# Performance work log

Hardware: AMD Instinct MI355X
Metric: run time of the kernel (lower is better)

## Reference

```python
import jax, jax.numpy as jnp
import numpy as np

B, N, D = 512, 256, 128
N_LAYER, N_HEAD = 4, 1
VAR = 0.01
HEAD = 0  # head_choice in run_mode=0


def setup_inputs() -> dict:
    key = jax.random.key(0)
    k1, k2 = jax.random.split(key)
    Z = jax.random.normal(k1, (B, N + 1, D + 1), dtype=jnp.float32)
    # allparam ~ N(0, var): torch .normal_(0, var) uses var as stddev
    allparam = jax.random.normal(k2, (N_LAYER, N_HEAD, 2, D, D), dtype=jnp.float32) * VAR
    gamma = jnp.ones((N_LAYER, N_HEAD, 1, N + 1, D + 1), dtype=jnp.float32)
    return {"Z": Z, "allparam": allparam, "gamma": gamma}


def _pad_full(M, corner):
    # Embed d x d matrix in (d+1) x (d+1) with zeros; set bottom-right corner.
    d = M.shape[0]
    full = jnp.zeros((d + 1, d + 1), M.dtype).at[:d, :d].set(M)
    return full.at[d, d].set(corner)


def _attention(P, Q, Z):
    # Z: [B, N+1, d+1]
    n = Z.shape[1] - 1
    P_full = _pad_full(P, 1.0)   # P with 1 at [d, d]
    Q_full = _pad_full(Q, 0.0)
    Attn = jnp.einsum('bni,ij,bmj->bnm', Z, Q_full, Z)  # [B, N+1, N+1]
    key = jnp.einsum('ij,bnj->bni', P_full, Z)           # [B, N+1, d+1]
    # A = eye(N+1) with A[N, N] = 0  <=>  zero the last token's key row
    key = key.at[:, n, :].set(0.0)
    return jnp.einsum('bnm,bmi->bni', Attn, key) / n


def reference(Z, allparam, gamma):
    # run_mode=0, chosen head = HEAD
    # T_i = R_i + sum_{k<i} R_k * gamma_k ; Z <- Z + T_i
    acc = jnp.zeros_like(Z)  # running sum_{k<i} R_k * gamma_k
    for i in range(N_LAYER):
        P = allparam[i, HEAD, 0]
        Q = allparam[i, HEAD, 1]
        R = _attention(P, Q, Z)
        T = R + acc
        acc = acc + R * gamma[i, HEAD, 0]
        Z = Z + T
    return Z
```

## Files before the change

kernel.cpp:

```cpp
#include <hip/hip_runtime.h>
#include <hip/hip_bf16.h>
#include <stdint.h>


using short8 = __attribute__((ext_vector_type(8))) short;
using f32x4  = __attribute__((ext_vector_type(4))) float;

#define MFMA16(A,B,C) __builtin_amdgcn_mfma_f32_16x16x32_bf16((A),(B),(C),0,0,0)

static __device__ __forceinline__ uint16_t f2bf(float f){
  union{__hip_bfloat16 h;uint16_t u;}c; c.h=__float2bfloat16(f); return c.u; }
static __device__ __forceinline__ uint32_t pk2(float lo,float hi){
  return (uint32_t)f2bf(lo) | ((uint32_t)f2bf(hi)<<16); }
static __device__ __forceinline__ float bfu(uint16_t u){ return __uint_as_float(((uint32_t)u)<<16); }
static __device__ __forceinline__ float bflo(uint32_t p){ return __uint_as_float(p<<16); }
static __device__ __forceinline__ float bfhi(uint32_t p){ return __uint_as_float(p&0xffff0000u); }

union F4 { uint32_t u[4]; short8 s8; };

#define ZTP   264
#define BUFP  152
#define SCRP  40
#define ZT_OFF   0
#define GBA_OFF  67584
#define GBB_OFF  106496
#define SCR_OFF  145408
#define ZBAR_OFF 155648
#define Z256_OFF 156688
#define A128_OFF 157200
#define A256_OFF 158224
#define G_OFF    158752
#define M1_OFF   159264
#define LDS_TOTAL 159776

__global__ __launch_bounds__(512)
__attribute__((amdgpu_waves_per_eu(2, 2)))
void tf_layers(const float* __restrict__ Zin, const float* __restrict__ gamma,
               const uint16_t* __restrict__ Qg, const uint16_t* __restrict__ Pg,
               float* __restrict__ Zout)
{
  extern __shared__ char lds[];
  uint16_t* ZT    = (uint16_t*)(lds + ZT_OFF);
  uint16_t* GbA   = (uint16_t*)(lds + GBA_OFF);
  uint16_t* GbB   = (uint16_t*)(lds + GBB_OFF);
  float*    zbar  = (float*)(lds + ZBAR_OFF);
  float*    z256f = (float*)(lds + Z256_OFF);
  float*    acc128= (float*)(lds + A128_OFF);
  float*    acc256= (float*)(lds + A256_OFF);
  float*    gv    = (float*)(lds + G_OFF);
  float*    m1v   = (float*)(lds + M1_OFF);

  const int tid = threadIdx.x, lane = tid & 63, w = tid >> 6;
  const int l15 = lane & 15, g4 = lane >> 4;
  const int b = blockIdx.x;
  const float inv_n = 1.0f/256.0f;

  uint16_t* scr = (uint16_t*)(lds + SCR_OFF) + w * 16 * SCRP;

  const float* Zb = Zin + (size_t)b*33153;
  float*       Zo = Zout + (size_t)b*33153;

  uint4* accb = (uint4*)(((uintptr_t)Zo + 15) & ~(uintptr_t)15);

  for (int i2 = tid; i2 < 33153; i2 += 512) {
    int r = i2/129, c = i2 - r*129;
    float v = Zb[i2];
    if (c < 128) { if (r < 256) ZT[c*ZTP + r] = f2bf(v); else z256f[c] = v; }
    else zbar[r] = v;
  }
  if (tid < 256) acc128[tid] = 0.0f;
  if (tid < 129) acc256[tid] = 0.0f;

  uint32_t lopk[2][16];
#pragma unroll
  for (int ti = 0; ti < 2; ++ti) {
    const int mb = 16*w + 128*ti;
#pragma unroll
    for (int it = 0; it < 8; ++it) {
      const float* zp = Zb + (size_t)(mb + 4*g4)*129 + 16*it + l15;
      float v0 = zp[0], v1 = zp[129], v2 = zp[258], v3 = zp[387];
      lopk[ti][2*it]   = pk2(v0 - bfu(f2bf(v0)), v1 - bfu(f2bf(v1)));
      lopk[ti][2*it+1] = pk2(v2 - bfu(f2bf(v2)), v3 - bfu(f2bf(v3)));
    }
  }

#pragma unroll 1
  for (int l = 0; l < 4; ++l) {
    const uint16_t* Ql  = Qg + l*16384;
    const uint16_t* Pl  = Pg + l*16384;
    const float*    gml = gamma + l*33153;
    const bool last = (l == 3);

    __syncthreads();

    {
      f32x4 gacc[8];
#pragma unroll
      for (int jt = 0; jt < 8; ++jt) gacc[jt] = (f32x4){0,0,0,0};
#pragma unroll
      for (int mw = 0; mw < 8; ++mw) {
        short8 af = *(const short8*)(ZT + (16*w+l15)*ZTP + 32*mw + 8*g4);
#pragma unroll
        for (int jt = 0; jt < 8; ++jt) {
          short8 bf = *(const short8*)(ZT + (16*jt+l15)*ZTP + 32*mw + 8*g4);
          gacc[jt] = MFMA16(af, bf, gacc[jt]);
        }
      }
#pragma unroll
      for (int jt = 0; jt < 8; ++jt)
        *(uint2*)(GbA + (16*jt+l15)*BUFP + 16*w + 4*g4) =
            make_uint2(pk2(gacc[jt][0],gacc[jt][1]), pk2(gacc[jt][2],gacc[jt][3]));
      {
        const int i = tid >> 2, q = lane & 3;
        float s = 0;
#pragma unroll
        for (int jj = 0; jj < 8; ++jj) {
          const int t0 = 8*q + 32*jj;
          uint4 zv = *(const uint4*)(ZT + i*ZTP + t0);
          f32x4 z0 = *(const f32x4*)(zbar + t0);
          f32x4 z1 = *(const f32x4*)(zbar + t0 + 4);
          s += bflo(zv.x)*z0[0] + bfhi(zv.x)*z0[1] + bflo(zv.y)*z0[2] + bfhi(zv.y)*z0[3]
             + bflo(zv.z)*z1[0] + bfhi(zv.z)*z1[1] + bflo(zv.w)*z1[2] + bfhi(zv.w)*z1[3];
        }
        s += __shfl_xor(s,1); s += __shfl_xor(s,2);
        if (q == 0) gv[i] = s;
      }
    }
    __syncthreads();

    uint32_t t1t[16];
    {
      short8 bq[4];
#pragma unroll
      for (int k = 0; k < 4; ++k)
        bq[k] = *(const short8*)(Pl + (16*w+l15)*128 + 32*k + 8*g4);
#pragma unroll
      for (int it = 0; it < 8; ++it) {
        f32x4 d4 = {0,0,0,0};
#pragma unroll
        for (int k = 0; k < 4; ++k) {
          short8 ag = *(const short8*)(GbA + (16*it+l15)*BUFP + 32*k + 8*g4);
          d4 = MFMA16(ag, bq[k], d4);
        }
        t1t[2*it]   = pk2(d4[0], d4[1]);
        t1t[2*it+1] = pk2(d4[2], d4[3]);
      }
      {
        const int d = tid >> 2, q = lane & 3;
        float s = 0;
#pragma unroll
        for (int j = 0; j < 4; ++j) {
          short8 qv = *(const short8*)(Ql + d*128 + 32*q + 8*j);
          f32x4 g0 = *(const f32x4*)(gv + 32*q + 8*j);
          f32x4 g1 = *(const f32x4*)(gv + 32*q + 8*j + 4);
          s += bfu((uint16_t)qv[0])*g0[0] + bfu((uint16_t)qv[1])*g0[1]
             + bfu((uint16_t)qv[2])*g0[2] + bfu((uint16_t)qv[3])*g0[3]
             + bfu((uint16_t)qv[4])*g1[0] + bfu((uint16_t)qv[5])*g1[1]
             + bfu((uint16_t)qv[6])*g1[2] + bfu((uint16_t)qv[7])*g1[3];
        }
        s += __shfl_xor(s,1); s += __shfl_xor(s,2);
        if (q == 0) m1v[d] = s;
      }
    }

    {
      F4 bfr[4];
#pragma unroll
      for (int k2 = 0; k2 < 4; ++k2) {
        *(uint2*)(scr + l15*SCRP + 4*g4)      = make_uint2(t1t[4*k2],   t1t[4*k2+1]);
        *(uint2*)(scr + l15*SCRP + 16 + 4*g4) = make_uint2(t1t[4*k2+2], t1t[4*k2+3]);
        bfr[k2].s8 = *(const short8*)(scr + l15*SCRP + 8*g4);
      }
#pragma unroll
      for (int dt = 0; dt < 8; ++dt) {
        f32x4 d4 = {0,0,0,0};
#pragma unroll
        for (int k2 = 0; k2 < 4; ++k2) {
          short8 aq = *(const short8*)(Ql + (16*dt+l15)*128 + 32*k2 + 8*g4);
          d4 = MFMA16(aq, bfr[k2].s8, d4);
        }
        *(uint2*)(GbB + (16*w+l15)*BUFP + 16*dt + 4*g4) =
            make_uint2(pk2(d4[0],d4[1]), pk2(d4[2],d4[3]));
      }
    }
    __syncthreads();

    float r256v = 0.0f, rcv = 0.0f;
#pragma unroll
    for (int ti = 0; ti < 2; ++ti) {
      const int mb = 16*w + 128*ti;
      F4 aw[4];
      float rp = 0;
#pragma unroll
      for (int q = 0; q < 4; ++q) {
        uint16_t ev[8];
#pragma unroll
        for (int j = 0; j < 8; ++j) ev[j] = ZT[(32*q + 8*g4 + j)*ZTP + mb + l15];
        aw[q].u[0] = (uint32_t)ev[0] | ((uint32_t)ev[1]<<16);
        aw[q].u[1] = (uint32_t)ev[2] | ((uint32_t)ev[3]<<16);
        aw[q].u[2] = (uint32_t)ev[4] | ((uint32_t)ev[5]<<16);
        aw[q].u[3] = (uint32_t)ev[6] | ((uint32_t)ev[7]<<16);
        f32x4 m0 = *(const f32x4*)(m1v + 32*q + 8*g4);
        f32x4 m4 = *(const f32x4*)(m1v + 32*q + 8*g4 + 4);
        rp += bfu(ev[0])*m0[0] + bfu(ev[1])*m0[1] + bfu(ev[2])*m0[2] + bfu(ev[3])*m0[3]
            + bfu(ev[4])*m4[0] + bfu(ev[5])*m4[1] + bfu(ev[6])*m4[2] + bfu(ev[7])*m4[3];
      }
      rp += __shfl_xor(rp,16); rp += __shfl_xor(rp,32);
      rp *= inv_n;
#pragma unroll
      for (int h = 0; h < 2; ++h) {
        uint4 q0, q1;
        if (l > 0) {
          q0 = accb[(((ti*2 + h)*2 + 0) << 9) + tid];
          q1 = accb[(((ti*2 + h)*2 + 1) << 9) + tid];
        } else {
          q0 = make_uint4(0,0,0,0); q1 = make_uint4(0,0,0,0);
        }
        f32x4 racc[4];
#pragma unroll
        for (int i = 0; i < 4; ++i) racc[i] = (f32x4){0,0,0,0};
#pragma unroll
        for (int c4 = 0; c4 < 4; ++c4) {
          const int ct = 4*h + c4;
#pragma unroll
          for (int q = 0; q < 4; ++q) {
            short8 bm = *(const short8*)(GbB + (16*ct+l15)*BUFP + 32*q + 8*g4);
            racc[c4] = MFMA16(aw[q].s8, bm, racc[c4]);
          }
        }
        uint32_t ao[8];
        ao[0]=q0.x; ao[1]=q0.y; ao[2]=q0.z; ao[3]=q0.w;
        ao[4]=q1.x; ao[5]=q1.y; ao[6]=q1.z; ao[7]=q1.w;
        uint32_t an[8];
#pragma unroll
        for (int c4 = 0; c4 < 4; ++c4) {
          const int ct = 4*h + c4;
          uint16_t* zt = ZT + (16*ct+l15)*ZTP + mb + 4*g4;
          uint2 hold = *(uint2*)zt;
          const float* gp = gml + (size_t)(mb + 4*g4)*129 + 16*ct + l15;
          float R0 = racc[c4][0]*inv_n, R1 = racc[c4][1]*inv_n;
          float R2 = racc[c4][2]*inv_n, R3 = racc[c4][3]*inv_n;
          float a0 = bflo(ao[2*c4]),   a1 = bfhi(ao[2*c4]);
          float a2 = bflo(ao[2*c4+1]), a3 = bfhi(ao[2*c4+1]);
          float z0 = bflo(hold.x) + bflo(lopk[ti][2*ct])   + R0 + a0;
          float z1 = bfhi(hold.x) + bfhi(lopk[ti][2*ct])   + R1 + a1;
          float z2 = bflo(hold.y) + bflo(lopk[ti][2*ct+1]) + R2 + a2;
          float z3 = bfhi(hold.y) + bfhi(lopk[ti][2*ct+1]) + R3 + a3;
          an[2*c4]   = pk2(a0 + R0*gp[0],   a1 + R1*gp[129]);
          an[2*c4+1] = pk2(a2 + R2*gp[258], a3 + R3*gp[387]);
          uint16_t h0 = f2bf(z0), h1 = f2bf(z1), h2 = f2bf(z2), h3 = f2bf(z3);
          *(uint2*)zt = make_uint2((uint32_t)h0 | ((uint32_t)h1<<16),
                                   (uint32_t)h2 | ((uint32_t)h3<<16));
          lopk[ti][2*ct]   = pk2(z0 - bfu(h0), z1 - bfu(h1));
          lopk[ti][2*ct+1] = pk2(z2 - bfu(h2), z3 - bfu(h3));
        }
        if (!last) {
          accb[(((ti*2 + h)*2 + 0) << 9) + tid] = make_uint4(an[0],an[1],an[2],an[3]);
          accb[(((ti*2 + h)*2 + 1) << 9) + tid] = make_uint4(an[4],an[5],an[6],an[7]);
        }
      }
      if (lane < 16) {
        const int m = mb + l15;
        float zb = zbar[m], a = acc128[m], ga = gml[m*129 + 128];
        float zn = zb + rp + a;
        zbar[m] = zn; acc128[m] = a + rp*ga;
      }
    }
    {
      const int c = tid >> 2, q = lane & 3;
      float s = 0;
#pragma unroll
      for (int jj = 0; jj < 4; ++jj) {
        const int d0 = 8*q + 32*jj;
        uint4 mv = *(const uint4*)(GbB + c*BUFP + d0);
        f32x4 z0 = *(const f32x4*)(z256f + d0);
        f32x4 z1 = *(const f32x4*)(z256f + d0 + 4);
        s += z0[0]*bflo(mv.x) + z0[1]*bfhi(mv.x) + z0[2]*bflo(mv.y) + z0[3]*bfhi(mv.y)
           + z1[0]*bflo(mv.z) + z1[1]*bfhi(mv.z) + z1[2]*bflo(mv.w) + z1[3]*bfhi(mv.w);
      }
      s += __shfl_xor(s,1); s += __shfl_xor(s,2);
      r256v = s;
    }
    if (w == 0) {
      const int d0 = lane*2;
      float s = z256f[d0]*m1v[d0] + z256f[d0+1]*m1v[d0+1];
      s += __shfl_xor(s,1); s += __shfl_xor(s,2); s += __shfl_xor(s,4);
      s += __shfl_xor(s,8); s += __shfl_xor(s,16); s += __shfl_xor(s,32);
      rcv = s;
    }
    __syncthreads();

    if ((lane & 3) == 0) {
      const int c = tid >> 2;
      float R = r256v*inv_n;
      float z = z256f[c], a = acc256[c], ga = gml[256*129 + c];
      float zn = z + R + a;
      z256f[c] = zn; acc256[c] = a + R*ga;
    }
    if (w == 0 && lane == 0) {
      float R = rcv*inv_n;
      float ga = gml[256*129 + 128];
      float zn = zbar[256] + R + acc256[128];
      zbar[256] = zn; acc256[128] = acc256[128] + R*ga;
    }
  }

  __syncthreads();
  for (int i2 = tid; i2 < 33153; i2 += 512) {
    int r = i2/129, c = i2 - r*129;
    float v;
    if (c < 128) v = (r == 256) ? z256f[c] : bfu(ZT[c*ZTP + r]);
    else         v = zbar[r];
    Zo[i2] = v;
  }
}

__global__ void prep_params(const float* __restrict__ ap,
                            uint16_t* __restrict__ qg, uint16_t* __restrict__ pg)
{
  int t = blockIdx.x * 256 + threadIdx.x;
  int l = t >> 14, rem = t & 16383;
  pg[t] = f2bf(ap[(l*2 + 0)*16384 + rem]);
  qg[t] = f2bf(ap[(l*2 + 1)*16384 + rem]);
}

extern "C" void kernel_launch(void* const* d_in, const int* in_sizes, int n_in,
                              void* d_out, int out_size, void* d_ws, size_t ws_size,
                              hipStream_t stream)
{
  const float* Z  = (const float*)d_in[0];
  const float* ap = (const float*)d_in[1];
  const float* gm = (const float*)d_in[2];

  uint16_t* qg = (uint16_t*)d_ws;
  uint16_t* pg = qg + 4*128*128;

  (void)hipFuncSetAttribute((const void*)tf_layers,
                            hipFuncAttributeMaxDynamicSharedMemorySize, LDS_TOTAL);

  prep_params<<<256, 256, 0, stream>>>(ap, qg, pg);
  tf_layers<<<512, 512, LDS_TOTAL, stream>>>(Z, gm, qg, pg, (float*)d_out);
}
```

Measured before the change: 254.0 us.

## Swizzle ZT LDS rows and pre-transpose gamma for coalesced vector loads

Replaces the fixed ZT row pitch with a padded index function that adds an 8-element skew every eight rows, meant to cut LDS bank conflicts on the column-wise strided reads. Adds a prep kernel that transposes gamma into a [layer][col][m] workspace layout, so the update loop fetches four gamma values with a single 16-byte load instead of four strided scalar loads. This costs an extra kernel launch and workspace traffic, and keeps a fallback path when the workspace is too small. It also hoists the per-layer top barrier out of the loop to a single barrier before it.

Result: slower. 292.3 us (+15.1%).

```diff
diff --git a/kernel.cpp b/kernel.cpp
--- a/kernel.cpp
+++ b/kernel.cpp
@@ -18,25 +18,27 @@
 
 union F4 { uint32_t u[4]; short8 s8; };
 
-#define ZTP   264
+static __device__ __forceinline__ int zto(int d){ return d*264 + (d & ~7); }
+
 #define BUFP  152
 #define SCRP  40
 #define ZT_OFF   0
-#define GBA_OFF  67584
-#define GBB_OFF  106496
-#define SCR_OFF  145408
-#define ZBAR_OFF 155648
-#define Z256_OFF 156688
-#define A128_OFF 157200
-#define A256_OFF 158224
-#define G_OFF    158752
-#define M1_OFF   159264
-#define LDS_TOTAL 159776
+#define GBA_OFF  67840
+#define GBB_OFF  106752
+#define SCR_OFF  145664
+#define ZBAR_OFF 155904
+#define Z256_OFF 156944
+#define A128_OFF 157456
+#define A256_OFF 158480
+#define G_OFF    159008
+#define M1_OFF   159520
+#define LDS_TOTAL 160032
 
 __global__ __launch_bounds__(512)
 __attribute__((amdgpu_waves_per_eu(2, 2)))
 void tf_layers(const float* __restrict__ Zin, const float* __restrict__ gamma,
                const uint16_t* __restrict__ Qg, const uint16_t* __restrict__ Pg,
+               const float* __restrict__ gt,
                float* __restrict__ Zout)
 {
   extern __shared__ char lds[];
@@ -65,7 +67,7 @@
   for (int i2 = tid; i2 < 33153; i2 += 512) {
     int r = i2/129, c = i2 - r*129;
     float v = Zb[i2];
-    if (c < 128) { if (r < 256) ZT[c*ZTP + r] = f2bf(v); else z256f[c] = v; }
+    if (c < 128) { if (r < 256) ZT[zto(c) + r] = f2bf(v); else z256f[c] = v; }
     else zbar[r] = v;
   }
   if (tid < 256) acc128[tid] = 0.0f;
@@ -83,15 +85,15 @@
       lopk[ti][2*it+1] = pk2(v2 - bfu(f2bf(v2)), v3 - bfu(f2bf(v3)));
     }
   }
+  __syncthreads();
 
 #pragma unroll 1
   for (int l = 0; l < 4; ++l) {
     const uint16_t* Ql  = Qg + l*16384;
     const uint16_t* Pl  = Pg + l*16384;
     const float*    gml = gamma + l*33153;
+    const float*    gtl = gt ? (gt + (size_t)l*129*260) : nullptr;
     const bool last = (l == 3);
-
-    __syncthreads();
 
     {
       f32x4 gacc[8];
@@ -99,10 +101,10 @@
       for (int jt = 0; jt < 8; ++jt) gacc[jt] = (f32x4){0,0,0,0};
 #pragma unroll
       for (int mw = 0; mw < 8; ++mw) {
-        short8 af = *(const short8*)(ZT + (16*w+l15)*ZTP + 32*mw + 8*g4);
+        short8 af = *(const short8*)(ZT + zto(16*w+l15) + 32*mw + 8*g4);
 #pragma unroll
         for (int jt = 0; jt < 8; ++jt) {
-          short8 bf = *(const short8*)(ZT + (16*jt+l15)*ZTP + 32*mw + 8*g4);
+          short8 bf = *(const short8*)(ZT + zto(16*jt+l15) + 32*mw + 8*g4);
           gacc[jt] = MFMA16(af, bf, gacc[jt]);
         }
       }
@@ -116,7 +118,7 @@
 #pragma unroll
         for (int jj = 0; jj < 8; ++jj) {
           const int t0 = 8*q + 32*jj;
-          uint4 zv = *(const uint4*)(ZT + i*ZTP + t0);
+          uint4 zv = *(const uint4*)(ZT + zto(i) + t0);
           f32x4 z0 = *(const f32x4*)(zbar + t0);
           f32x4 z1 = *(const f32x4*)(zbar + t0 + 4);
           s += bflo(zv.x)*z0[0] + bfhi(zv.x)*z0[1] + bflo(zv.y)*z0[2] + bfhi(zv.y)*z0[3]
@@ -195,7 +197,7 @@
       for (int q = 0; q < 4; ++q) {
         uint16_t ev[8];
 #pragma unroll
-        for (int j = 0; j < 8; ++j) ev[j] = ZT[(32*q + 8*g4 + j)*ZTP + mb + l15];
+        for (int j = 0; j < 8; ++j) ev[j] = ZT[zto(32*q + 8*g4 + j) + mb + l15];
         aw[q].u[0] = (uint32_t)ev[0] | ((uint32_t)ev[1]<<16);
         aw[q].u[1] = (uint32_t)ev[2] | ((uint32_t)ev[3]<<16);
         aw[q].u[2] = (uint32_t)ev[4] | ((uint32_t)ev[5]<<16);
@@ -234,10 +236,17 @@
         uint32_t an[8];
 #pragma unroll
         for (int c4 = 0; c4 < 4; ++c4) {
-          const int ct = 4*h + c4;
-          uint16_t* zt = ZT + (16*ct+l15)*ZTP + mb + 4*g4;
+          const int ct = 4*h + c4, col = 16*ct + l15;
+          uint16_t* zt = ZT + zto(col) + mb + 4*g4;
           uint2 hold = *(uint2*)zt;
-          const float* gp = gml + (size_t)(mb + 4*g4)*129 + 16*ct + l15;
+          float ga0, ga1, ga2, ga3;
+          if (gtl) {
+            f32x4 g4v = *(const f32x4*)(gtl + (size_t)col*260 + mb + 4*g4);
+            ga0 = g4v[0]; ga1 = g4v[1]; ga2 = g4v[2]; ga3 = g4v[3];
+          } else {
+            const float* gp = gml + (size_t)(mb + 4*g4)*129 + col;
+            ga0 = gp[0]; ga1 = gp[129]; ga2 = gp[258]; ga3 = gp[387];
+          }
           float R0 = racc[c4][0]*inv_n, R1 = racc[c4][1]*inv_n;
           float R2 = racc[c4][2]*inv_n, R3 = racc[c4][3]*inv_n;
           float a0 = bflo(ao[2*c4]),   a1 = bfhi(ao[2*c4]);
@@ -246,8 +255,8 @@
           float z1 = bfhi(hold.x) + bfhi(lopk[ti][2*ct])   + R1 + a1;
           float z2 = bflo(hold.y) + bflo(lopk[ti][2*ct+1]) + R2 + a2;
           float z3 = bfhi(hold.y) + bfhi(lopk[ti][2*ct+1]) + R3 + a3;
-          an[2*c4]   = pk2(a0 + R0*gp[0],   a1 + R1*gp[129]);
-          an[2*c4+1] = pk2(a2 + R2*gp[258], a3 + R3*gp[387]);
+          an[2*c4]   = pk2(a0 + R0*ga0, a1 + R1*ga1);
+          an[2*c4+1] = pk2(a2 + R2*ga2, a3 + R3*ga3);
           uint16_t h0 = f2bf(z0), h1 = f2bf(z1), h2 = f2bf(z2), h3 = f2bf(z3);
           *(uint2*)zt = make_uint2((uint32_t)h0 | ((uint32_t)h1<<16),
                                    (uint32_t)h2 | ((uint32_t)h3<<16));
@@ -309,7 +318,7 @@
   for (int i2 = tid; i2 < 33153; i2 += 512) {
     int r = i2/129, c = i2 - r*129;
     float v;
-    if (c < 128) v = (r == 256) ? z256f[c] : bfu(ZT[c*ZTP + r]);
+    if (c < 128) v = (r == 256) ? z256f[c] : bfu(ZT[zto(c) + r]);
     else         v = zbar[r];
     Zo[i2] = v;
   }
@@ -324,6 +333,15 @@
   qg[t] = f2bf(ap[(l*2 + 1)*16384 + rem]);
 }
 
+__global__ void prep_gt(const float* __restrict__ gm, float* __restrict__ gt)
+{
+  int t = blockIdx.x * 256 + threadIdx.x;
+  if (t >= 4*129*257) return;
+  int l = t / 33153, rem = t - l*33153;
+  int c = rem / 257, m = rem - c*257;
+  gt[((size_t)l*129 + c)*260 + m] = gm[(size_t)l*33153 + m*129 + c];
+}
+
 extern "C" void kernel_launch(void* const* d_in, const int* in_sizes, int n_in,
                               void* d_out, int out_size, void* d_ws, size_t ws_size,
                               hipStream_t stream)
@@ -335,9 +353,13 @@
   uint16_t* qg = (uint16_t*)d_ws;
   uint16_t* pg = qg + 4*128*128;
 
+  const size_t gt_need = 262144 + (size_t)4*129*260*4;
+  float* gt = (ws_size >= gt_need) ? (float*)((char*)d_ws + 262144) : nullptr;
+
   (void)hipFuncSetAttribute((const void*)tf_layers,
                             hipFuncAttributeMaxDynamicSharedMemorySize, LDS_TOTAL);
 
   prep_params<<<256, 256, 0, stream>>>(ap, qg, pg);
-  tf_layers<<<512, 512, LDS_TOTAL, stream>>>(Z, gm, qg, pg, (float*)d_out);
+  if (gt) prep_gt<<<519, 256, 0, stream>>>(gm, gt);
+  tf_layers<<<512, 512, LDS_TOTAL, stream>>>(Z, gm, qg, pg, gt, (float*)d_out);
 }
```
